# Performance work log

Measured on AMD Instinct MI355X. Metric: run time of the kernel, lower is better.

Reference implementation:

```python
import jax, jax.numpy as jnp
import numpy as np

B, S, D, H = 4, 2048, 1024, 16
HD = D // H


def setup_inputs() -> dict:
    key = jax.random.key(0)
    ks = jax.random.split(key, 9)
    s = 1.0 / np.sqrt(D)
    return {
        "x": jax.random.normal(ks[0], (B, S, D), dtype=jnp.float32),
        "Wq": jax.random.normal(ks[1], (D, D), dtype=jnp.float32) * s,
        "bq": jnp.zeros((D,), dtype=jnp.float32),
        "Wk": jax.random.normal(ks[2], (D, D), dtype=jnp.float32) * s,
        "bk": jnp.zeros((D,), dtype=jnp.float32),
        "Wv": jax.random.normal(ks[3], (D, D), dtype=jnp.float32) * s,
        "bv": jnp.zeros((D,), dtype=jnp.float32),
        "Wo": jax.random.normal(ks[4], (D, D), dtype=jnp.float32) * s,
        "bo": jnp.zeros((D,), dtype=jnp.float32),
    }


def reference(x, Wq, bq, Wk, bk, Wv, bv, Wo, bo):
    b, s, d = x.shape
    # project and split heads -> [b, h, s, hd]
    def split_heads(t):
        return t.reshape(b, s, H, HD).transpose(0, 2, 1, 3)
    q = split_heads(x @ Wq.T + bq)
    k = split_heads(x @ Wk.T + bk)
    v = split_heads(x @ Wv.T + bv)
    scale = 1.0 / np.sqrt(HD).astype(np.float32)
    att = jnp.einsum('bhqd,bhkd->bhqk', q, k) * scale
    causal = jnp.tril(jnp.ones((s, s), dtype=bool))
    att = jnp.where(causal[None, None], att, -jnp.inf)
    att = jax.nn.softmax(att, axis=-1)
    out = jnp.einsum('bhqk,bhkd->bhqd', att, v)  # [b,h,s,hd]
    out = out.transpose(0, 2, 1, 3).reshape(b, s, d)
    return out @ Wo.T + bo
```

## Files before the change

kernel.cpp:

```cpp
#include <hip/hip_runtime.h>
#include <hip/hip_bf16.h>
#include <math.h>

typedef __hip_bfloat16 bf16;
typedef __attribute__((ext_vector_type(8))) __bf16 bf16x8;
typedef __attribute__((ext_vector_type(4))) float f32x4;

__device__ __forceinline__ void gload_lds16(const void* g, void* l) {
  __builtin_amdgcn_global_load_lds(
      (const __attribute__((address_space(1))) unsigned int*)g,
      (__attribute__((address_space(3))) unsigned int*)l, 16, 0, 0);
}

__global__ void cvt_bf16(const float* __restrict__ in, bf16* __restrict__ out, int n) {
  int idx = (blockIdx.x * blockDim.x + threadIdx.x) * 8;
  if (idx >= n) return;
  float4 v0 = *(const float4*)(in + idx);
  float4 v1 = *(const float4*)(in + idx + 4);
  alignas(16) bf16 tmp[8];
  tmp[0] = __float2bfloat16(v0.x); tmp[1] = __float2bfloat16(v0.y);
  tmp[2] = __float2bfloat16(v0.z); tmp[3] = __float2bfloat16(v0.w);
  tmp[4] = __float2bfloat16(v1.x); tmp[5] = __float2bfloat16(v1.y);
  tmp[6] = __float2bfloat16(v1.z); tmp[7] = __float2bfloat16(v1.w);
  *(uint4*)(out + idx) = *(const uint4*)tmp;
}

__global__ void prep_w(const float* __restrict__ Wq, const float* __restrict__ Wk,
                       const float* __restrict__ Wv, const float* __restrict__ Wo,
                       const float* __restrict__ bq, const float* __restrict__ bk,
                       const float* __restrict__ bv,
                       bf16* __restrict__ wqkv, bf16* __restrict__ wo16,
                       float* __restrict__ b3) {
  const float QSCL = 0.125f * 1.4426950408889634f;
  const int bi = blockIdx.x;
  if (bi < 2048) {
    const int seg = bi >> 9;
    const int idx = ((bi & 511) * 256 + threadIdx.x) * 8;
    const float* src = seg == 0 ? Wq : seg == 1 ? Wk : seg == 2 ? Wv : Wo;
    bf16* dst = seg < 3 ? wqkv + (size_t)seg * 1048576 : wo16;
    const float m = (seg == 0) ? QSCL : 1.0f;
    float4 v0 = *(const float4*)(src + idx);
    float4 v1 = *(const float4*)(src + idx + 4);
    alignas(16) bf16 tmp[8];
    tmp[0] = __float2bfloat16(v0.x * m); tmp[1] = __float2bfloat16(v0.y * m);
    tmp[2] = __float2bfloat16(v0.z * m); tmp[3] = __float2bfloat16(v0.w * m);
    tmp[4] = __float2bfloat16(v1.x * m); tmp[5] = __float2bfloat16(v1.y * m);
    tmp[6] = __float2bfloat16(v1.z * m); tmp[7] = __float2bfloat16(v1.w * m);
    *(uint4*)(dst + idx) = *(const uint4*)tmp;
  } else {
    const int i = (bi - 2048) * 256 + threadIdx.x;
    if (i < 3072)
      b3[i] = i < 1024 ? bq[i] * QSCL : i < 2048 ? bk[i - 1024] : bv[i - 2048];
  }
}

template<int MODE>
__global__ __launch_bounds__(512, 2) void gemm3(
    const bf16* __restrict__ A, const bf16* __restrict__ Bw,
    const float* __restrict__ bias, void* __restrict__ Cout,
    bf16* __restrict__ vt, int N, int K)
{
  constexpr int SLOT = 24576;
  __shared__ bf16 lds[3 * SLOT];
  const int tid = threadIdx.x;
  const int wave = tid >> 6, lane = tid & 63;
  const int lhi = lane >> 4, llo = lane & 15;
  const int wr = wave >> 2, wc = wave & 3;

  const int xcd = blockIdx.x & 7;
  const int l = blockIdx.x >> 3;
  const int row0 = (xcd * 8 + (l & 7)) * 128;
  const int col0 = (l >> 3) * 256;

  auto stageA = [&](int t) {
    bf16* s = &lds[(t % 3) * SLOT];
    const size_t k0 = (size_t)t << 6;
#pragma unroll
    for (int j = 0; j < 2; ++j) {
      int i = j * 512 + tid;
      int r = i >> 3, gl = (i & 7) ^ (r & 7);
      gload_lds16(A + (size_t)(row0 + r) * K + k0 + gl * 8, s + i * 8);
    }
  };
  auto stageBh = [&](int t, int half) {
    bf16* s = &lds[(t % 3) * SLOT] + 8192;
    const size_t k0 = (size_t)t << 6;
#pragma unroll
    for (int j = 0; j < 2; ++j) {
      int i = half * 1024 + j * 512 + tid;
      int r = i >> 3, gl = (i & 7) ^ (r & 7);
      gload_lds16(Bw + (size_t)(col0 + r) * K + k0 + gl * 8, s + i * 8);
    }
  };

  f32x4 acc[4][4] = {};
  const int T = K >> 6;

  stageA(0); stageBh(0, 0); stageBh(0, 1);
  stageA(1); stageBh(1, 0); stageBh(1, 1);
  asm volatile("s_waitcnt vmcnt(6)" ::: "memory");
  __builtin_amdgcn_s_barrier();

  for (int t = 0; t < T; ++t) {
    const bf16* sa = &lds[(t % 3) * SLOT];
    const bf16* sb = sa + 8192;

    bf16x8 af[4][2], bfr[2][2];
#pragma unroll
    for (int m = 0; m < 4; ++m)
#pragma unroll
      for (int kk = 0; kk < 2; ++kk) {
        int r = wr * 64 + m * 16 + llo;
        af[m][kk] = *(const bf16x8*)&sa[r * 64 + (((kk * 4 + lhi) ^ (r & 7)) << 3)];
      }
#pragma unroll
    for (int n = 0; n < 2; ++n)
#pragma unroll
      for (int kk = 0; kk < 2; ++kk) {
        int c = wc * 64 + n * 16 + llo;
        bfr[n][kk] = *(const bf16x8*)&sb[c * 64 + (((kk * 4 + lhi) ^ (c & 7)) << 3)];
      }
    if (t + 2 < T) { stageA(t + 2); stageBh(t + 2, 0); }
    __builtin_amdgcn_s_barrier();
    __builtin_amdgcn_s_setprio(1);
#pragma unroll
    for (int m = 0; m < 4; ++m)
#pragma unroll
      for (int n = 0; n < 2; ++n)
#pragma unroll
        for (int kk = 0; kk < 2; ++kk)
          acc[m][n] = __builtin_amdgcn_mfma_f32_16x16x32_bf16(af[m][kk], bfr[n][kk], acc[m][n], 0, 0, 0);
    __builtin_amdgcn_s_setprio(0);
    __builtin_amdgcn_s_barrier();

#pragma unroll
    for (int n = 0; n < 2; ++n)
#pragma unroll
      for (int kk = 0; kk < 2; ++kk) {
        int c = wc * 64 + 32 + n * 16 + llo;
        bfr[n][kk] = *(const bf16x8*)&sb[c * 64 + (((kk * 4 + lhi) ^ (c & 7)) << 3)];
      }
    if (t + 2 < T) stageBh(t + 2, 1);
    __builtin_amdgcn_s_barrier();
    __builtin_amdgcn_s_setprio(1);
#pragma unroll
    for (int m = 0; m < 4; ++m)
#pragma unroll
      for (int n = 0; n < 2; ++n)
#pragma unroll
        for (int kk = 0; kk < 2; ++kk)
          acc[m][2 + n] = __builtin_amdgcn_mfma_f32_16x16x32_bf16(af[m][kk], bfr[n][kk], acc[m][2 + n], 0, 0, 0);
    __builtin_amdgcn_s_setprio(0);
    if (t + 2 < T)      asm volatile("s_waitcnt vmcnt(6)" ::: "memory");
    else if (t + 1 < T) asm volatile("s_waitcnt vmcnt(0)" ::: "memory");
    __builtin_amdgcn_s_barrier();
  }

#pragma unroll
  for (int m = 0; m < 4; ++m)
#pragma unroll
    for (int n = 0; n < 4; ++n) {
      const int col = col0 + wc * 64 + (n & 1) * 16 + (n >> 1) * 32 + llo;
      const float bv = bias[col];
      const int rowbase = row0 + wr * 64 + m * 16 + lhi * 4;
      if (MODE == 1) {
#pragma unroll
        for (int j = 0; j < 4; ++j)
          ((float*)Cout)[(size_t)(rowbase + j) * N + col] = acc[m][n][j] + bv;
      } else if (col < 2048) {
#pragma unroll
        for (int j = 0; j < 4; ++j)
          ((bf16*)Cout)[(size_t)(rowbase + j) * N + col] = __float2bfloat16(acc[m][n][j] + bv);
      } else {
        const int hh = (col - 2048) >> 6, d = (col - 2048) & 63;
        const int bb = rowbase >> 11, s0 = rowbase & 2047;
        alignas(8) bf16 tmp[4];
#pragma unroll
        for (int j = 0; j < 4; ++j) tmp[j] = __float2bfloat16(acc[m][n][j] + bv);
        *(uint2*)&vt[((size_t)(bb * 16 + hh) * 64 + d) * 2048 + s0] = *(const uint2*)tmp;
      }
    }
}

__global__ __launch_bounds__(512, 4) void attn(
    const bf16* __restrict__ QKV, const bf16* __restrict__ Vt,
    bf16* __restrict__ O)
{
  const int S = 2048, DM = 3072;
  const int bx = blockIdx.x;
  const int qt = (bx < 256) ? (bx >> 6) : (7 - ((bx - 256) >> 6));
  const int rem = bx & 63, h = rem >> 2, b = rem & 3;
  const int tid = threadIdx.x, wave = tid >> 6, lane = tid & 63;
  const int lhi = lane >> 4, llo = lane & 15;

  __shared__ bf16 lK[2][64 * 64];
  __shared__ bf16 lV[2][64 * 64];
  __shared__ bf16 lP[8][32 * 64];

  const size_t rowb = (size_t)b * S;
  const int q0 = qt * 256;
  const int nkt = 4 * qt + 4;
  const int qw = q0 + wave * 32;
  const int dmax = (qw + 31) >> 6;

  bf16x8 vones;
#pragma unroll
  for (int i = 0; i < 8; ++i) vones[i] = (__bf16)1.0f;

  auto stageKV = [&](int buf, int kt) {
    const int i = tid;
    const int r = i >> 3;
    const int ce = ((i & 7) * 8) ^ ((r & 7) << 3);
    gload_lds16(&QKV[(rowb + (size_t)kt * 64 + r) * DM + 1024 + h * 64 + ce],
                &lK[buf][i * 8]);
    gload_lds16(&Vt[((size_t)(b * 16 + h) * 64 + r) * S + kt * 64 + ce],
                &lV[buf][i * 8]);
  };

  bf16x8 qf[2][2];
#pragma unroll
  for (int hh = 0; hh < 2; ++hh)
#pragma unroll
    for (int kk = 0; kk < 2; ++kk)
      qf[hh][kk] = *(const bf16x8*)&QKV[(rowb + qw + hh * 16 + llo) * DM
                                        + h * 64 + kk * 32 + lhi * 8];

  f32x4 o_acc[2][4] = {};
  f32x4 o_l[2] = {};

  stageKV(0, 0);
  for (int kt = 0; kt < nkt; ++kt) {
    __syncthreads();
    if (kt + 1 < nkt) stageKV((kt + 1) & 1, kt + 1);
    if (kt > dmax) continue;
    const int buf = kt & 1;

    f32x4 s[2][4] = {};
    __builtin_amdgcn_s_setprio(1);
#pragma unroll
    for (int kk = 0; kk < 2; ++kk)
#pragma unroll
      for (int n = 0; n < 4; ++n) {
        const int kr = n * 16 + llo;
        bf16x8 kf = *(const bf16x8*)&lK[buf][kr * 64 + ((kk * 32 + lhi * 8) ^ ((kr & 7) << 3))];
        s[0][n] = __builtin_amdgcn_mfma_f32_16x16x32_bf16(kf, qf[0][kk], s[0][n], 0, 0, 0);
        s[1][n] = __builtin_amdgcn_mfma_f32_16x16x32_bf16(kf, qf[1][kk], s[1][n], 0, 0, 0);
      }
    __builtin_amdgcn_s_setprio(0);

#pragma unroll
    for (int hh = 0; hh < 2; ++hh) {
      if (kt >= ((qw + hh * 16) >> 6)) {
        const int lim = qw + hh * 16 + llo - kt * 64;
#pragma unroll
        for (int n = 0; n < 4; ++n)
#pragma unroll
          for (int j = 0; j < 4; ++j)
            if (n * 16 + lhi * 4 + j > lim) s[hh][n][j] = -INFINITY;
      }

#pragma unroll
      for (int n = 0; n < 4; ++n)
#pragma unroll
        for (int j = 0; j < 4; ++j)
          s[hh][n][j] = exp2f(s[hh][n][j]);

#pragma unroll
      for (int n = 0; n < 4; ++n) {
        alignas(8) bf16 tmp[4];
#pragma unroll
        for (int j = 0; j < 4; ++j) tmp[j] = __float2bfloat16(s[hh][n][j]);
        const int g = (n * 4 + lhi) ^ ((llo & 7) << 1);
        *(uint2*)&lP[wave][(hh * 16 + llo) * 64 + g * 4] = *(const uint2*)tmp;
      }
    }

    __builtin_amdgcn_s_setprio(1);
#pragma unroll
    for (int kk = 0; kk < 2; ++kk) {
      const int g0 = (kk * 8 + lhi * 2) ^ ((llo & 7) << 1);
      bf16x8 pf0 = *(const bf16x8*)&lP[wave][(llo) * 64 + g0 * 4];
      bf16x8 pf1 = *(const bf16x8*)&lP[wave][(16 + llo) * 64 + g0 * 4];
#pragma unroll
      for (int n = 0; n < 4; ++n) {
        const int vr = n * 16 + llo;
        bf16x8 vf = *(const bf16x8*)&lV[buf][vr * 64 + ((kk * 32 + lhi * 8) ^ ((vr & 7) << 3))];
        o_acc[0][n] = __builtin_amdgcn_mfma_f32_16x16x32_bf16(vf, pf0, o_acc[0][n], 0, 0, 0);
        o_acc[1][n] = __builtin_amdgcn_mfma_f32_16x16x32_bf16(vf, pf1, o_acc[1][n], 0, 0, 0);
      }
      o_l[0] = __builtin_amdgcn_mfma_f32_16x16x32_bf16(vones, pf0, o_l[0], 0, 0, 0);
      o_l[1] = __builtin_amdgcn_mfma_f32_16x16x32_bf16(vones, pf1, o_l[1], 0, 0, 0);
    }
    __builtin_amdgcn_s_setprio(0);
  }

#pragma unroll
  for (int hh = 0; hh < 2; ++hh) {
    const float inv = 1.0f / o_l[hh][0];
    const size_t orow = (rowb + qw + hh * 16 + llo) * 1024 + h * 64;
#pragma unroll
    for (int n = 0; n < 4; ++n) {
      alignas(8) bf16 tmp[4];
#pragma unroll
      for (int j = 0; j < 4; ++j) tmp[j] = __float2bfloat16(o_acc[hh][n][j] * inv);
      *(uint2*)&O[orow + n * 16 + lhi * 4] = *(const uint2*)tmp;
    }
  }
}

extern "C" void kernel_launch(void* const* d_in, const int* in_sizes, int n_in,
                              void* d_out, int out_size, void* d_ws, size_t ws_size,
                              hipStream_t stream) {
  const float* x  = (const float*)d_in[0];
  const float* Wq = (const float*)d_in[1];
  const float* bq = (const float*)d_in[2];
  const float* Wk = (const float*)d_in[3];
  const float* bk = (const float*)d_in[4];
  const float* Wv = (const float*)d_in[5];
  const float* bv = (const float*)d_in[6];
  const float* Wo = (const float*)d_in[7];
  const float* bo = (const float*)d_in[8];

  const int Bb = 4, S = 2048, D = 1024;
  const int M = Bb * S;
  const int N3 = 3 * D;

  bf16* x16  = (bf16*)d_ws;
  bf16* wqkv = x16 + (size_t)M * D;
  bf16* wo16 = wqkv + (size_t)3 * D * D;
  bf16* qkv  = wo16 + (size_t)D * D;
  bf16* vt   = qkv + (size_t)M * N3;
  float* b3  = (float*)(vt + (size_t)M * D);
  size_t needed = ((size_t)M * D * 3 + 4 * (size_t)D * D + (size_t)M * N3) * 2 + 3072 * 4;
  if (ws_size < needed) return;

  cvt_bf16<<<(M * D) / (8 * 256), 256, 0, stream>>>(x, x16, M * D);
  prep_w<<<2060, 256, 0, stream>>>(Wq, Wk, Wv, Wo, bq, bk, bv, wqkv, wo16, b3);

  gemm3<0><<<(M / 128) * (N3 / 256), 512, 0, stream>>>(x16, wqkv, b3, qkv, vt, N3, D);
  attn<<<dim3(512, 1, 1), 512, 0, stream>>>(qkv, vt, x16);
  gemm3<1><<<(M / 128) * (D / 256), 512, 0, stream>>>(x16, wo16, bo, d_out, nullptr, D, D);
}
```

Measured before the change: 174.6 us.

## Software-pipeline attention so PV of previous tile overlaps QK of current

```diff
diff --git a/kernel.cpp b/kernel.cpp
--- a/kernel.cpp
+++ b/kernel.cpp
@@ -194,7 +194,7 @@
   const int lhi = lane >> 4, llo = lane & 15;
 
   __shared__ bf16 lK[2][64 * 64];
-  __shared__ bf16 lV[2][64 * 64];
+  __shared__ bf16 lV[3][64 * 64];
   __shared__ bf16 lP[8][32 * 64];
 
   const size_t rowb = (size_t)b * S;
@@ -207,14 +207,19 @@
 #pragma unroll
   for (int i = 0; i < 8; ++i) vones[i] = (__bf16)1.0f;
 
-  auto stageKV = [&](int buf, int kt) {
+  auto stageK = [&](int buf, int kt) {
     const int i = tid;
     const int r = i >> 3;
     const int ce = ((i & 7) * 8) ^ ((r & 7) << 3);
     gload_lds16(&QKV[(rowb + (size_t)kt * 64 + r) * DM + 1024 + h * 64 + ce],
                 &lK[buf][i * 8]);
+  };
+  auto stageV = [&](int slot, int kt) {
+    const int i = tid;
+    const int r = i >> 3;
+    const int ce = ((i & 7) * 8) ^ ((r & 7) << 3);
     gload_lds16(&Vt[((size_t)(b * 16 + h) * 64 + r) * S + kt * 64 + ce],
-                &lV[buf][i * 8]);
+                &lV[slot][i * 8]);
   };
 
   bf16x8 qf[2][2];
@@ -228,53 +233,8 @@
   f32x4 o_acc[2][4] = {};
   f32x4 o_l[2] = {};
 
-  stageKV(0, 0);
-  for (int kt = 0; kt < nkt; ++kt) {
-    __syncthreads();
-    if (kt + 1 < nkt) stageKV((kt + 1) & 1, kt + 1);
-    if (kt > dmax) continue;
-    const int buf = kt & 1;
-
-    f32x4 s[2][4] = {};
-    __builtin_amdgcn_s_setprio(1);
-#pragma unroll
-    for (int kk = 0; kk < 2; ++kk)
-#pragma unroll
-      for (int n = 0; n < 4; ++n) {
-        const int kr = n * 16 + llo;
-        bf16x8 kf = *(const bf16x8*)&lK[buf][kr * 64 + ((kk * 32 + lhi * 8) ^ ((kr & 7) << 3))];
-        s[0][n] = __builtin_amdgcn_mfma_f32_16x16x32_bf16(kf, qf[0][kk], s[0][n], 0, 0, 0);
-        s[1][n] = __builtin_amdgcn_mfma_f32_16x16x32_bf16(kf, qf[1][kk], s[1][n], 0, 0, 0);
-      }
-    __builtin_amdgcn_s_setprio(0);
-
-#pragma unroll
-    for (int hh = 0; hh < 2; ++hh) {
-      if (kt >= ((qw + hh * 16) >> 6)) {
-        const int lim = qw + hh * 16 + llo - kt * 64;
-#pragma unroll
-        for (int n = 0; n < 4; ++n)
-#pragma unroll
-          for (int j = 0; j < 4; ++j)
-            if (n * 16 + lhi * 4 + j > lim) s[hh][n][j] = -INFINITY;
-      }
-
-#pragma unroll
-      for (int n = 0; n < 4; ++n)
-#pragma unroll
-        for (int j = 0; j < 4; ++j)
-          s[hh][n][j] = exp2f(s[hh][n][j]);
-
-#pragma unroll
-      for (int n = 0; n < 4; ++n) {
-        alignas(8) bf16 tmp[4];
-#pragma unroll
-        for (int j = 0; j < 4; ++j) tmp[j] = __float2bfloat16(s[hh][n][j]);
-        const int g = (n * 4 + lhi) ^ ((llo & 7) << 1);
-        *(uint2*)&lP[wave][(hh * 16 + llo) * 64 + g * 4] = *(const uint2*)tmp;
-      }
-    }
-
+  auto pv_tile = [&](int pvt) {
+    const int vb = pvt % 3;
     __builtin_amdgcn_s_setprio(1);
 #pragma unroll
     for (int kk = 0; kk < 2; ++kk) {
@@ -284,7 +244,7 @@
 #pragma unroll
       for (int n = 0; n < 4; ++n) {
         const int vr = n * 16 + llo;
-        bf16x8 vf = *(const bf16x8*)&lV[buf][vr * 64 + ((kk * 32 + lhi * 8) ^ ((vr & 7) << 3))];
+        bf16x8 vf = *(const bf16x8*)&lV[vb][vr * 64 + ((kk * 32 + lhi * 8) ^ ((vr & 7) << 3))];
         o_acc[0][n] = __builtin_amdgcn_mfma_f32_16x16x32_bf16(vf, pf0, o_acc[0][n], 0, 0, 0);
         o_acc[1][n] = __builtin_amdgcn_mfma_f32_16x16x32_bf16(vf, pf1, o_acc[1][n], 0, 0, 0);
       }
@@ -292,7 +252,69 @@
       o_l[1] = __builtin_amdgcn_mfma_f32_16x16x32_bf16(vones, pf1, o_l[1], 0, 0, 0);
     }
     __builtin_amdgcn_s_setprio(0);
+  };
+
+  stageK(0, 0); stageV(0, 0);
+  asm volatile("s_waitcnt vmcnt(1)" ::: "memory");
+  __builtin_amdgcn_s_barrier();
+
+  for (int kt = 0; kt < nkt; ++kt) {
+    if (kt > 0) {
+      asm volatile("s_waitcnt vmcnt(1)" ::: "memory");
+      __builtin_amdgcn_s_barrier();
+    }
+    if (kt + 1 < nkt) { stageK((kt + 1) & 1, kt + 1); stageV((kt + 1) % 3, kt + 1); }
+
+    const int pvt = kt - 1;
+    if (pvt >= 0 && pvt <= dmax) pv_tile(pvt);
+
+    if (kt <= dmax) {
+      const int buf = kt & 1;
+      f32x4 s[2][4] = {};
+      __builtin_amdgcn_s_setprio(1);
+#pragma unroll
+      for (int kk = 0; kk < 2; ++kk)
+#pragma unroll
+        for (int n = 0; n < 4; ++n) {
+          const int kr = n * 16 + llo;
+          bf16x8 kf = *(const bf16x8*)&lK[buf][kr * 64 + ((kk * 32 + lhi * 8) ^ ((kr & 7) << 3))];
+          s[0][n] = __builtin_amdgcn_mfma_f32_16x16x32_bf16(kf, qf[0][kk], s[0][n], 0, 0, 0);
+          s[1][n] = __builtin_amdgcn_mfma_f32_16x16x32_bf16(kf, qf[1][kk], s[1][n], 0, 0, 0);
+        }
+      __builtin_amdgcn_s_setprio(0);
+
+#pragma unroll
+      for (int hh = 0; hh < 2; ++hh) {
+        if (kt >= ((qw + hh * 16) >> 6)) {
+          const int lim = qw + hh * 16 + llo - kt * 64;
+#pragma unroll
+          for (int n = 0; n < 4; ++n)
+#pragma unroll
+            for (int j = 0; j < 4; ++j)
+              if (n * 16 + lhi * 4 + j > lim) s[hh][n][j] = -INFINITY;
+        }
+
+#pragma unroll
+        for (int n = 0; n < 4; ++n)
+#pragma unroll
+          for (int j = 0; j < 4; ++j)
+            s[hh][n][j] = exp2f(s[hh][n][j]);
+
+#pragma unroll
+        for (int n = 0; n < 4; ++n) {
+          alignas(8) bf16 tmp[4];
+#pragma unroll
+          for (int j = 0; j < 4; ++j) tmp[j] = __float2bfloat16(s[hh][n][j]);
+          const int g = (n * 4 + lhi) ^ ((llo & 7) << 1);
+          *(uint2*)&lP[wave][(hh * 16 + llo) * 64 + g * 4] = *(const uint2*)tmp;
+        }
+      }
+    }
   }
+
+  asm volatile("s_waitcnt vmcnt(0)" ::: "memory");
+  __builtin_amdgcn_s_barrier();
+  if (dmax == nkt - 1) pv_tile(nkt - 1);
 
 #pragma unroll
   for (int hh = 0; hh < 2; ++hh) {
```

Measured after the change: 190.2 us. 1.09x slower.
